# Optimization experiments

Measured on AMD Instinct MI355X. Metric: run time of the kernel, lower is better.

## Reference

```python
import jax, jax.numpy as jnp
import numpy as np

NUM_TAG = 9
B, S = 4096, 512


def setup_inputs() -> dict:
    key = jax.random.key(0)
    k1, k2, k3, k4 = jax.random.split(key, 4)
    bert_encode = jax.random.normal(k1, (B, S, NUM_TAG), dtype=jnp.float32)
    # variable-length contiguous prefix masks (as the torch code assumes via features[mask==1])
    lengths = jax.random.randint(k2, (B,), 1, S + 1)
    output_mask = (jnp.arange(S)[None, :] < lengths[:, None]).astype(jnp.int32)
    tags = jax.random.randint(k3, (B, S), 0, NUM_TAG).astype(jnp.int64)
    # transitions: (num_tag+2, num_tag+2), uniform(-0.1, 0.1), end row / start col = -10000
    t = jax.random.uniform(k4, (NUM_TAG + 2, NUM_TAG + 2), minval=-0.1, maxval=0.1, dtype=jnp.float32)
    t = t.at[NUM_TAG + 1, :].set(-10000.0).at[:, NUM_TAG].set(-10000.0)
    return {"bert_encode": bert_encode, "output_mask": output_mask, "tags": tags, "transitions": t}


def _crf_nll(bert_encode, transitions, output_mask, tags):
    ntag = bert_encode.shape[-1]
    start, end = ntag, ntag + 1
    maskf = output_mask.astype(bert_encode.dtype)              # (B, S)
    lengths = output_mask.sum(-1)                              # (B,)
    # ---- real path score (vectorized over batch) ----
    emit = jnp.take_along_axis(bert_encode, tags[..., None], axis=-1)[..., 0]  # (B, S)
    emit_score = (emit * maskf).sum(-1)
    first_trans = transitions[start, tags[:, 0]]
    mid = transitions[tags[:, :-1], tags[:, 1:]]               # (B, S-1)
    mid_score = (mid * maskf[:, 1:]).sum(-1)
    last_tag = jnp.take_along_axis(tags, (lengths - 1)[:, None], axis=1)[:, 0]
    last_trans = transitions[last_tag, end]
    real = emit_score + first_trans + mid_score + last_trans   # (B,)
    # ---- all-possible-path score: forward algorithm via scan over time ----
    trans_tt = transitions[:ntag, :ntag]                       # (ntag, ntag)
    alpha0 = transitions[start, :ntag][None, :] + bert_encode[:, 0, :]  # (B, ntag)

    def step(alpha, xs):
        em, m = xs                                             # (B, ntag), (B,)
        new = jax.nn.logsumexp(alpha[:, :, None] + trans_tt[None, :, :] + em[:, None, :], axis=1)
        return jnp.where(m[:, None] > 0, new, alpha), None

    em_seq = jnp.swapaxes(bert_encode[:, 1:, :], 0, 1)         # (S-1, B, ntag)
    m_seq = jnp.swapaxes(output_mask[:, 1:], 0, 1)             # (S-1, B)
    alpha, _ = jax.lax.scan(step, alpha0, (em_seq, m_seq))
    total = jax.nn.logsumexp(alpha + transitions[:ntag, end][None, :], axis=-1)  # (B,)
    num_chars = maskf.sum()
    return jnp.sum(total - real) / num_chars


def reference(bert_encode, output_mask, tags, transitions):
    return _crf_nll(bert_encode, transitions, output_mask, tags)
```

## Files before the change

kernel.cpp:

```cpp
#include <hip/hip_runtime.h>

#define LOG2E 1.4426950408889634f
#define LN2   0.6931471805599453f

#if __has_builtin(__builtin_amdgcn_exp2f)
#define EXP2(x) __builtin_amdgcn_exp2f(x)
#else
#define EXP2(x) exp2f(x)
#endif
#if __has_builtin(__builtin_amdgcn_logf)
#define LOG2(x) __builtin_amdgcn_logf(x)
#else
#define LOG2(x) log2f(x)
#endif

constexpr int BB = 4096;
constexpr int S  = 512;
constexpr int NT = 9;
constexpr int TD = 11;
constexpr int PF = 16;

__global__ __launch_bounds__(256) void crf_fused(
    const float* __restrict__ em,
    const int*   __restrict__ mask,
    const int*   __restrict__ tags,
    const float* __restrict__ trans,
    float* __restrict__ blkV,
    float* __restrict__ blkN)
{
    __shared__ float s_val[16];
    __shared__ float s_n[16];

    const int tid = threadIdx.x;
    const int g   = tid >> 4;
    const int k   = tid & 15;
    const int b   = blockIdx.x * 16 + g;

    const float* emB   = em + (size_t)b * (S * NT);
    const int*   maskB = mask + b * S;
    const int*   tagsB = tags + b * S;

    float sumE = 0.f;
    int   cnt  = 0;

    int t  = k;
    int mk = maskB[t];
    int tg = tagsB[t];
    int prevcarry = 0;

    float p_gv = 0.f, p_tr = 0.f;
    int   p_mk = 0;

    for (int i = 0; i < S / 16; ++i) {
        int mk2 = 0, tg2 = 0;
        if (i + 1 < S / 16) {
            mk2 = maskB[t + 16];
            tg2 = tagsB[t + 16];
        }
        float gv  = emB[t * NT + tg];
        int   tgp = __shfl_up(tg, 1, 16);
        if (k == 0) tgp = prevcarry;
        float tr  = (t > 0) ? trans[tgp * TD + tg] : 0.f;
        prevcarry = __shfl(tg, 15, 16);

        if (p_mk) { sumE += p_gv + p_tr; cnt++; }
        p_gv = gv; p_tr = tr; p_mk = mk;

        mk = mk2; tg = tg2; t += 16;
    }
    if (p_mk) { sumE += p_gv + p_tr; cnt++; }

    #pragma unroll
    for (int d = 1; d < 16; d <<= 1) {
        sumE += __shfl_xor(sumE, d, 16);
        cnt  += __shfl_xor(cnt,  d, 16);
    }
    const int L = cnt;

    if (k == 0) {
        int tg0 = tagsB[0];
        int tgl = tagsB[L - 1];
        sumE += trans[9 * TD + tg0] + trans[tgl * TD + 10];
        s_val[g] = -sumE;
        s_n[g]   = (float)L;
    }

    int Lw = L;
    Lw = max(Lw, __shfl_xor(Lw, 16));
    Lw = max(Lw, __shfl_xor(Lw, 32));

    const bool active = (k < NT);
    const int  j = active ? k : 0;

    float w[NT];
    #pragma unroll
    for (int i = 0; i < NT; ++i)
        w[i] = EXP2(trans[i * TD + j] * LOG2E);

    float a = (trans[9 * TD + j] + emB[j]) * LOG2E;
    if (!active) a = -1e30f;
    float m = a;
    #pragma unroll
    for (int d = 1; d < 16; d <<= 1) m = fmaxf(m, __shfl_xor(m, d, 16));
    float e = active ? EXP2(a - m) : 0.f;

    float pf[PF];
    #pragma unroll
    for (int i = 0; i < PF; ++i) {
        int tt  = 1 + i;
        int idx = tt < S ? tt : S - 1;
        pf[i] = emB[idx * NT + j];
    }

    for (int base = 1; base < Lw; base += PF) {
        float nx[PF];
        #pragma unroll
        for (int i = 0; i < PF; ++i) {
            int tt  = base + PF + i;
            int idx = tt < S ? tt : S - 1;
            nx[i] = emB[idx * NT + j];
        }
        #pragma unroll
        for (int i = 0; i < PF; ++i) {
            const int tt = base + i;
            float emc = pf[i] * LOG2E;

            float e0 = __shfl(e, 0, 16);
            float e1 = __shfl(e, 1, 16);
            float e2 = __shfl(e, 2, 16);
            float e3 = __shfl(e, 3, 16);
            float e4 = __shfl(e, 4, 16);
            float e5 = __shfl(e, 5, 16);
            float e6 = __shfl(e, 6, 16);
            float e7 = __shfl(e, 7, 16);
            float e8 = __shfl(e, 8, 16);

            float d0 = e0 * w[0];
            d0 = fmaf(e1, w[1], d0);
            d0 = fmaf(e2, w[2], d0);
            float d1 = e3 * w[3];
            d1 = fmaf(e4, w[4], d1);
            d1 = fmaf(e5, w[5], d1);
            float d2 = e6 * w[6];
            d2 = fmaf(e7, w[7], d2);
            d2 = fmaf(e8, w[8], d2);
            float dot = (d0 + d1) + d2;

            float anew = emc + m + LOG2(dot);
            if (active && tt < L) a = anew;
            if ((i & 3) == 3) m = m + LOG2(e0);
            e = active ? EXP2(a - m) : 0.f;
        }
        #pragma unroll
        for (int i = 0; i < PF; ++i) pf[i] = nx[i];
    }

    float v  = active ? (a + trans[j * TD + 10] * LOG2E) : -1e30f;
    float m2 = v;
    #pragma unroll
    for (int d = 1; d < 16; d <<= 1) m2 = fmaxf(m2, __shfl_xor(m2, d, 16));
    float sv = active ? EXP2(v - m2) : 0.f;
    #pragma unroll
    for (int d = 1; d < 16; d <<= 1) sv += __shfl_xor(sv, d, 16);

    if (k == 0) {
        float total = (m2 + LOG2(sv)) * LN2;
        s_val[g] += total;
    }
    __syncthreads();
    if (tid == 0) {
        float vv = 0.f, nn = 0.f;
        #pragma unroll
        for (int q = 0; q < 16; ++q) { vv += s_val[q]; nn += s_n[q]; }
        blkV[blockIdx.x] = vv;
        blkN[blockIdx.x] = nn;
    }
}

__global__ __launch_bounds__(256) void crf_final(
    const float* __restrict__ blkV,
    const float* __restrict__ blkN,
    float* __restrict__ out)
{
    const int tid = threadIdx.x;
    float v = blkV[tid];
    float n = blkN[tid];
    #pragma unroll
    for (int d = 1; d < 64; d <<= 1) {
        v += __shfl_xor(v, d);
        n += __shfl_xor(n, d);
    }
    __shared__ float sv[4], sn[4];
    if ((tid & 63) == 0) { sv[tid >> 6] = v; sn[tid >> 6] = n; }
    __syncthreads();
    if (tid == 0) {
        float vv = sv[0] + sv[1] + sv[2] + sv[3];
        float nn = sn[0] + sn[1] + sn[2] + sn[3];
        out[0] = vv / nn;
    }
}

extern "C" void kernel_launch(void* const* d_in, const int* in_sizes, int n_in,
                              void* d_out, int out_size, void* d_ws, size_t ws_size,
                              hipStream_t stream) {
    const float* em    = (const float*)d_in[0];
    const int*   mask  = (const int*)d_in[1];
    const int*   tags  = (const int*)d_in[2];
    const float* trans = (const float*)d_in[3];
    float* blkV = (float*)d_ws;
    float* blkN = blkV + 256;

    crf_fused<<<BB / 16, 256, 0, stream>>>(em, mask, tags, trans, blkV, blkN);
    crf_final<<<1, 256, 0, stream>>>(blkV, blkN, (float*)d_out);
}
```

Baseline: 186.9 us.

## Assign one wavefront per sequence with LDS double-buffered emissions and readlane broadcasts

Each 64-lane wavefront now handles a single batch row instead of four rows per wave with 16 lanes each. Emissions are staged through coalesced 64-step chunks into double-buffered shared memory. The recurrence uses scalar readlane broadcasts and renormalises against lane 0 at every step, so the cross-lane shuffle max is gone. This gives fewer sequences per wave (4x more blocks) and higher per-sequence latency exposure, in exchange for coalesced loads and cheaper broadcasts. Lanes 9-63 sit idle during the serial scan.

After: 221.1 us. 18.3% more time.

```diff
diff --git a/kernel.cpp b/kernel.cpp
--- a/kernel.cpp
+++ b/kernel.cpp
@@ -18,7 +18,12 @@
 constexpr int S  = 512;
 constexpr int NT = 9;
 constexpr int TD = 11;
-constexpr int PF = 16;
+constexpr int CH = 64;
+constexpr int CF = CH * NT;
+
+__device__ __forceinline__ float rdlane(float v, int l) {
+    return __uint_as_float(__builtin_amdgcn_readlane(__float_as_uint(v), l));
+}
 
 __global__ __launch_bounds__(256) void crf_fused(
     const float* __restrict__ em,
@@ -28,115 +33,94 @@
     float* __restrict__ blkV,
     float* __restrict__ blkN)
 {
-    __shared__ float s_val[16];
-    __shared__ float s_n[16];
+    __shared__ float sm[4][2][CF];
+    __shared__ float s_val[4];
+    __shared__ float s_n[4];
 
     const int tid = threadIdx.x;
-    const int g   = tid >> 4;
-    const int k   = tid & 15;
-    const int b   = blockIdx.x * 16 + g;
+    const int wv_id = tid >> 6;
+    const int l     = tid & 63;
+    const int b     = blockIdx.x * 4 + wv_id;
 
     const float* emB   = em + (size_t)b * (S * NT);
     const int*   maskB = mask + b * S;
     const int*   tagsB = tags + b * S;
 
+    float pf[9];
+    #pragma unroll
+    for (int r = 0; r < 9; ++r) pf[r] = emB[r * 64 + l];
+
     float sumE = 0.f;
     int   cnt  = 0;
-
-    int t  = k;
-    int mk = maskB[t];
-    int tg = tagsB[t];
-    int prevcarry = 0;
-
-    float p_gv = 0.f, p_tr = 0.f;
-    int   p_mk = 0;
-
-    for (int i = 0; i < S / 16; ++i) {
-        int mk2 = 0, tg2 = 0;
-        if (i + 1 < S / 16) {
-            mk2 = maskB[t + 16];
-            tg2 = tagsB[t + 16];
-        }
-        float gv  = emB[t * NT + tg];
-        int   tgp = __shfl_up(tg, 1, 16);
-        if (k == 0) tgp = prevcarry;
-        float tr  = (t > 0) ? trans[tgp * TD + tg] : 0.f;
-        prevcarry = __shfl(tg, 15, 16);
-
-        if (p_mk) { sumE += p_gv + p_tr; cnt++; }
-        p_gv = gv; p_tr = tr; p_mk = mk;
-
-        mk = mk2; tg = tg2; t += 16;
-    }
-    if (p_mk) { sumE += p_gv + p_tr; cnt++; }
-
-    #pragma unroll
-    for (int d = 1; d < 16; d <<= 1) {
-        sumE += __shfl_xor(sumE, d, 16);
-        cnt  += __shfl_xor(cnt,  d, 16);
+    int   prevcarry = 0;
+
+    #pragma unroll 2
+    for (int i = 0; i < S / 64; ++i) {
+        int   t  = i * 64 + l;
+        int   mk = maskB[t];
+        int   tg = tagsB[t];
+        float gv = emB[t * NT + tg];
+        int   tgp = __shfl_up(tg, 1);
+        if (l == 0) tgp = prevcarry;
+        float tr = (t > 0) ? trans[tgp * TD + tg] : 0.f;
+        prevcarry = __shfl(tg, 63);
+        if (mk) { sumE += gv + tr; cnt++; }
+    }
+    #pragma unroll
+    for (int d = 1; d < 64; d <<= 1) {
+        sumE += __shfl_xor(sumE, d);
+        cnt  += __shfl_xor(cnt, d);
     }
     const int L = cnt;
 
-    if (k == 0) {
+    if (l == 0) {
         int tg0 = tagsB[0];
         int tgl = tagsB[L - 1];
         sumE += trans[9 * TD + tg0] + trans[tgl * TD + 10];
-        s_val[g] = -sumE;
-        s_n[g]   = (float)L;
-    }
-
-    int Lw = L;
-    Lw = max(Lw, __shfl_xor(Lw, 16));
-    Lw = max(Lw, __shfl_xor(Lw, 32));
-
-    const bool active = (k < NT);
-    const int  j = active ? k : 0;
+    }
+
+    const bool active = (l < NT);
+    const int  jj = active ? l : 0;
 
     float w[NT];
     #pragma unroll
     for (int i = 0; i < NT; ++i)
-        w[i] = EXP2(trans[i * TD + j] * LOG2E);
-
-    float a = (trans[9 * TD + j] + emB[j]) * LOG2E;
+        w[i] = EXP2(trans[i * TD + jj] * LOG2E);
+
+    float a = (trans[9 * TD + jj] + emB[jj]) * LOG2E;
     if (!active) a = -1e30f;
-    float m = a;
-    #pragma unroll
-    for (int d = 1; d < 16; d <<= 1) m = fmaxf(m, __shfl_xor(m, d, 16));
+    float m = rdlane(a, 0);
     float e = active ? EXP2(a - m) : 0.f;
 
-    float pf[PF];
-    #pragma unroll
-    for (int i = 0; i < PF; ++i) {
-        int tt  = 1 + i;
-        int idx = tt < S ? tt : S - 1;
-        pf[i] = emB[idx * NT + j];
-    }
-
-    for (int base = 1; base < Lw; base += PF) {
-        float nx[PF];
+    #pragma unroll
+    for (int r = 0; r < 9; ++r) sm[wv_id][0][r * 64 + l] = pf[r];
+
+    for (int c = 0; c * CH < L; ++c) {
+        int cn = c + 1;
+        if (cn > S / CH - 1) cn = S / CH - 1;
         #pragma unroll
-        for (int i = 0; i < PF; ++i) {
-            int tt  = base + PF + i;
-            int idx = tt < S ? tt : S - 1;
-            nx[i] = emB[idx * NT + j];
-        }
-        #pragma unroll
-        for (int i = 0; i < PF; ++i) {
-            const int tt = base + i;
-            float emc = pf[i] * LOG2E;
-
-            float e0 = __shfl(e, 0, 16);
-            float e1 = __shfl(e, 1, 16);
-            float e2 = __shfl(e, 2, 16);
-            float e3 = __shfl(e, 3, 16);
-            float e4 = __shfl(e, 4, 16);
-            float e5 = __shfl(e, 5, 16);
-            float e6 = __shfl(e, 6, 16);
-            float e7 = __shfl(e, 7, 16);
-            float e8 = __shfl(e, 8, 16);
-
-            float d0 = e0 * w[0];
-            d0 = fmaf(e1, w[1], d0);
+        for (int r = 0; r < 9; ++r)
+            pf[r] = emB[cn * CF + r * 64 + l];
+
+        const float* buf = sm[wv_id][c & 1];
+        const int base = c * CH;
+        int t0 = base < 1 ? 1 : base;
+        int t1 = base + CH; if (t1 > L) t1 = L;
+
+        #pragma unroll 4
+        for (int tt = t0; tt < t1; ++tt) {
+            float emv = buf[(tt - base) * NT + jj];
+
+            float e1 = rdlane(e, 1);
+            float e2 = rdlane(e, 2);
+            float e3 = rdlane(e, 3);
+            float e4 = rdlane(e, 4);
+            float e5 = rdlane(e, 5);
+            float e6 = rdlane(e, 6);
+            float e7 = rdlane(e, 7);
+            float e8 = rdlane(e, 8);
+
+            float d0 = fmaf(e1, w[1], w[0]);
             d0 = fmaf(e2, w[2], d0);
             float d1 = e3 * w[3];
             d1 = fmaf(e4, w[4], d1);
@@ -146,16 +130,18 @@
             d2 = fmaf(e8, w[8], d2);
             float dot = (d0 + d1) + d2;
 
-            float anew = emc + m + LOG2(dot);
-            if (active && tt < L) a = anew;
-            if ((i & 3) == 3) m = m + LOG2(e0);
-            e = active ? EXP2(a - m) : 0.f;
+            float anew = fmaf(emv, LOG2E, m) + LOG2(dot);
+            a = active ? anew : a;
+            m = rdlane(a, 0);
+            e = EXP2(a - m);
         }
+
         #pragma unroll
-        for (int i = 0; i < PF; ++i) pf[i] = nx[i];
-    }
-
-    float v  = active ? (a + trans[j * TD + 10] * LOG2E) : -1e30f;
+        for (int r = 0; r < 9; ++r)
+            sm[wv_id][cn & 1][r * 64 + l] = pf[r];
+    }
+
+    float v  = active ? (a + trans[jj * TD + 10] * LOG2E) : -1e30f;
     float m2 = v;
     #pragma unroll
     for (int d = 1; d < 16; d <<= 1) m2 = fmaxf(m2, __shfl_xor(m2, d, 16));
@@ -163,17 +149,15 @@
     #pragma unroll
     for (int d = 1; d < 16; d <<= 1) sv += __shfl_xor(sv, d, 16);
 
-    if (k == 0) {
+    if (l == 0) {
         float total = (m2 + LOG2(sv)) * LN2;
-        s_val[g] += total;
+        s_val[wv_id] = total - sumE;
+        s_n[wv_id]   = (float)L;
     }
     __syncthreads();
     if (tid == 0) {
-        float vv = 0.f, nn = 0.f;
-        #pragma unroll
-        for (int q = 0; q < 16; ++q) { vv += s_val[q]; nn += s_n[q]; }
-        blkV[blockIdx.x] = vv;
-        blkN[blockIdx.x] = nn;
+        blkV[blockIdx.x] = s_val[0] + s_val[1] + s_val[2] + s_val[3];
+        blkN[blockIdx.x] = s_n[0] + s_n[1] + s_n[2] + s_n[3];
     }
 }
 
@@ -183,8 +167,12 @@
     float* __restrict__ out)
 {
     const int tid = threadIdx.x;
-    float v = blkV[tid];
-    float n = blkN[tid];
+    float v = 0.f, n = 0.f;
+    #pragma unroll
+    for (int i = 0; i < 4; ++i) {
+        v += blkV[tid + i * 256];
+        n += blkN[tid + i * 256];
+    }
     #pragma unroll
     for (int d = 1; d < 64; d <<= 1) {
         v += __shfl_xor(v, d);
@@ -194,9 +182,8 @@
     if ((tid & 63) == 0) { sv[tid >> 6] = v; sn[tid >> 6] = n; }
     __syncthreads();
     if (tid == 0) {
-        float vv = sv[0] + sv[1] + sv[2] + sv[3];
-        float nn = sn[0] + sn[1] + sn[2] + sn[3];
-        out[0] = vv / nn;
+        out[0] = (sv[0] + sv[1] + sv[2] + sv[3]) /
+                 (sn[0] + sn[1] + sn[2] + sn[3]);
     }
 }
 
@@ -208,8 +195,8 @@
     const int*   tags  = (const int*)d_in[2];
     const float* trans = (const float*)d_in[3];
     float* blkV = (float*)d_ws;
-    float* blkN = blkV + 256;
-
-    crf_fused<<<BB / 16, 256, 0, stream>>>(em, mask, tags, trans, blkV, blkN);
+    float* blkN = blkV + 1024;
+
+    crf_fused<<<BB / 4, 256, 0, stream>>>(em, mask, tags, trans, blkV, blkN);
     crf_final<<<1, 256, 0, stream>>>(blkV, blkN, (float*)d_out);
 }
```
